# Kernel optimization log

Hardware: AMD Instinct MI355X
Metric: run time of the kernel (lower is better)

The kernel has to match this reference:

```python
import jax, jax.numpy as jnp
import numpy as np

LN_EPS = 1e-5


def setup_inputs() -> dict:
    key = jax.random.key(0)
    k1, k2, k3, k4, k5 = jax.random.split(key, 5)
    V, D_REAL, D_HID, D_MODEL = 32000, 768, 512, 4096
    B, S = 4, 2048
    return {
        "real": jax.random.normal(k1, (V, D_REAL), dtype=jnp.float32),
        "llama_embed": jax.random.normal(k2, (V, D_MODEL), dtype=jnp.float32),
        "w1": jax.random.normal(k3, (D_HID, D_REAL), dtype=jnp.float32),  # trans_1.weight
        "w2": jax.random.normal(k4, (D_MODEL, D_HID), dtype=jnp.float32),  # trans_2.weight
        "ln_w": jnp.ones((D_HID,), dtype=jnp.float32),
        "ln_b": jnp.zeros((D_HID,), dtype=jnp.float32),
        "input_ids": jax.random.randint(k5, (B, S), 0, V, dtype=jnp.int64),
    }


def _layernorm(x, w, b):
    mu = jnp.mean(x, axis=-1, keepdims=True)
    var = jnp.mean(jnp.square(x - mu), axis=-1, keepdims=True)
    return (x - mu) * jax.lax.rsqrt(var + LN_EPS) * w + b


def reference(real, llama_embed, w1, w2, ln_w, ln_b, input_ids):
    # trans_2(ELU(LayerNorm(trans_1(real)))) over the FULL table, as in the original
    h = jnp.einsum("vd,hd->vh", real, w1)            # [V, 512]
    h = jax.nn.elu(_layernorm(h, ln_w, ln_b))        # [V, 512]
    transfered = jnp.einsum("vh,mh->vm", h, w2)      # [V, 4096]
    # gather rows per token and add frozen llama embeddings
    return transfered[input_ids] + llama_embed[input_ids]  # [B, S, 4096]
```

## Files before the change

kernel.cpp:

```cpp
#include <hip/hip_runtime.h>
#include <hip/hip_bf16.h>
#include <math.h>

#define TOKENS 8192
#define D_REAL 768
#define D_HID  512
#define D_MODEL 4096

typedef __attribute__((ext_vector_type(8))) short bf16x8;
typedef __attribute__((ext_vector_type(4))) float f32x4;

__device__ inline unsigned short f2bf(float f) {
    union { float f; unsigned u; } v; v.f = f;
    unsigned r = v.u + 0x7FFFu + ((v.u >> 16) & 1u);
    return (unsigned short)(r >> 16);
}
__device__ inline float bf2f(unsigned short h) {
    union { unsigned u; float f; } v; v.u = ((unsigned)h) << 16;
    return v.f;
}
__device__ inline bf16x8 cvt8(float4 a, float4 b) {
    bf16x8 r;
    r[0] = (short)f2bf(a.x); r[1] = (short)f2bf(a.y);
    r[2] = (short)f2bf(a.z); r[3] = (short)f2bf(a.w);
    r[4] = (short)f2bf(b.x); r[5] = (short)f2bf(b.y);
    r[6] = (short)f2bf(b.z); r[7] = (short)f2bf(b.w);
    return r;
}

__device__ inline void gload_lds16(const void* g, void* lds_wave_base) {
    __builtin_amdgcn_global_load_lds(
        (const __attribute__((address_space(1))) unsigned*)g,
        (__attribute__((address_space(3))) unsigned*)lds_wave_base,
        16, 0, 0);
}

__device__ inline void BAR() {
    asm volatile("" ::: "memory");
    __builtin_amdgcn_s_barrier();
    asm volatile("" ::: "memory");
}

__global__ __launch_bounds__(256)
void gemm1_mfma(const float* __restrict__ real, const int* __restrict__ ids,
                const unsigned short* __restrict__ B,
                unsigned short* __restrict__ C)
{
    constexpr int K = D_REAL, N = D_HID;
    __shared__ __align__(16) unsigned short As[64 * 32];
    __shared__ __align__(16) unsigned short Bs[128 * 32];
    __shared__ int sIds[64];

    const int tid = threadIdx.x;
    const int rowBase = blockIdx.x * 64;
    const int colBase = blockIdx.y * 128;

    if (tid < 64) sIds[tid] = ids[rowBase + tid];
    __syncthreads();

    const int srow = tid >> 2;
    const int scol = (tid & 3) * 8;
    const float* gA = real + (size_t)sIds[srow] * K + scol;
    const unsigned short* gB = B + (size_t)(colBase + srow) * K + scol;
    unsigned short* lB = Bs + (tid >> 6) * 512;

    const int lane = tid & 63;
    const int wv   = tid >> 6;
    const int wm   = (wv >> 1) * 32;
    const int wn   = (wv & 1) * 64;
    const int frow = lane & 15;
    const int fk   = (lane >> 4) * 8;

    f32x4 acc[2][4];
    #pragma unroll
    for (int i = 0; i < 2; i++)
        #pragma unroll
        for (int j = 0; j < 4; j++) acc[i][j] = (f32x4)0.f;

    for (int k0 = 0; k0 < K; k0 += 32) {
        gload_lds16(gB + k0,                lB);
        gload_lds16(gB + k0 + (size_t)64*K, lB + 2048);
        const float4 a0 = *reinterpret_cast<const float4*>(gA + k0);
        const float4 a1 = *reinterpret_cast<const float4*>(gA + k0 + 4);
        *reinterpret_cast<bf16x8*>(&As[srow * 32 + scol]) = cvt8(a0, a1);
        __syncthreads();

        bf16x8 af[2], bg[4];
        #pragma unroll
        for (int i = 0; i < 2; i++)
            af[i] = *reinterpret_cast<const bf16x8*>(&As[(wm + i*16 + frow) * 32 + fk]);
        #pragma unroll
        for (int j = 0; j < 4; j++)
            bg[j] = *reinterpret_cast<const bf16x8*>(&Bs[(wn + j*16 + frow) * 32 + fk]);

        #pragma unroll
        for (int i = 0; i < 2; i++)
            #pragma unroll
            for (int j = 0; j < 4; j++)
                acc[i][j] = __builtin_amdgcn_mfma_f32_16x16x32_bf16(af[i], bg[j], acc[i][j], 0, 0, 0);
        __syncthreads();
    }

    const int orow0 = wm + (lane >> 4) * 4;
    const int ocol0 = wn + frow;
    #pragma unroll
    for (int i = 0; i < 2; i++)
        #pragma unroll
        for (int r = 0; r < 4; r++) {
            unsigned short* dst = C + (size_t)(rowBase + orow0 + i*16 + r) * N + colBase + ocol0;
            #pragma unroll
            for (int j = 0; j < 4; j++)
                dst[j * 16] = f2bf(acc[i][j][r]);
        }
}

__global__ __launch_bounds__(512, 4)
void gemm2_mfma(const unsigned short* __restrict__ A,
                const unsigned short* __restrict__ B,
                const int* __restrict__ ids,
                const float* __restrict__ embed,
                float* __restrict__ C)
{
    constexpr int K = D_HID, N = D_MODEL, NKT = K / 64;
    __shared__ __align__(16) unsigned short lds2[32768];
    __shared__ int sIds[128];
    unsigned short* Alds = lds2;
    unsigned short* Blds = lds2 + 16384;

    const int f   = blockIdx.x;
    const int xcd = f & 7;
    const int idx = f >> 3;
    const int rowBase = (xcd * 8 + (idx & 7)) * 128;
    const int colBase = (idx >> 3) * 128;

    const int tid  = threadIdx.x;
    const int lane = tid & 63;
    const int wv   = tid >> 6;
    const int wr   = wv >> 2;
    const int wc   = wv & 3;
    const int frow = lane & 15;
    const int fq   = lane >> 4;

    if (tid < 128) sIds[tid] = ids[rowBase + tid];

    auto STAGE = [&](const unsigned short* Mp, unsigned short* Ml,
                     int tileBase, int kt) {
        if (kt >= NKT) return;
        unsigned short* Mb = Ml + (kt & 1) * 8192;
        #pragma unroll
        for (int u = 0; u < 2; ++u) {
            const int c    = u * 512 + tid;
            const int row  = c >> 3;
            const int slot = (c & 7) ^ (row & 7);
            const unsigned short* g = Mp + (size_t)(tileBase + row) * K
                                         + kt * 64 + slot * 8;
            gload_lds16(g, Mb + (u * 512 + wv * 64) * 8);
        }
    };
    auto LDA = [&](int buf, int mf, int kk) -> bf16x8 {
        const int row  = wr * 64 + mf * 16 + frow;
        const int slot = (kk * 4 + fq) ^ (row & 7);
        return *reinterpret_cast<const bf16x8*>(Alds + buf * 8192 + row * 64 + slot * 8);
    };
    auto LDB = [&](int buf, int nf, int kk) -> bf16x8 {
        const int row  = wc * 32 + nf * 16 + frow;
        const int slot = (kk * 4 + fq) ^ (row & 7);
        return *reinterpret_cast<const bf16x8*>(Blds + buf * 8192 + row * 64 + slot * 8);
    };

    f32x4 acc[4][2];
    #pragma unroll
    for (int i = 0; i < 4; i++)
        #pragma unroll
        for (int j = 0; j < 2; j++) acc[i][j] = (f32x4)0.f;

    STAGE(A, Alds, rowBase, 0);
    STAGE(B, Blds, colBase, 0);
    STAGE(A, Alds, rowBase, 1);
    asm volatile("s_waitcnt vmcnt(2)" ::: "memory");
    __builtin_amdgcn_s_barrier();
    asm volatile("" ::: "memory");

    #pragma unroll
    for (int kt = 0; kt < NKT; ++kt) {
        const int buf = kt & 1;
        bf16x8 af0[2][2], bg[2][2];
        #pragma unroll
        for (int i = 0; i < 2; ++i)
            #pragma unroll
            for (int kk = 0; kk < 2; ++kk)
                af0[i][kk] = LDA(buf, i, kk);
        #pragma unroll
        for (int nf = 0; nf < 2; ++nf)
            #pragma unroll
            for (int kk = 0; kk < 2; ++kk)
                bg[nf][kk] = LDB(buf, nf, kk);
        STAGE(B, Blds, colBase, kt + 1);
        BAR();
        __builtin_amdgcn_s_setprio(1);
        #pragma unroll
        for (int i = 0; i < 2; ++i)
            #pragma unroll
            for (int nf = 0; nf < 2; ++nf)
                #pragma unroll
                for (int kk = 0; kk < 2; ++kk)
                    acc[i][nf] = __builtin_amdgcn_mfma_f32_16x16x32_bf16(
                        af0[i][kk], bg[nf][kk], acc[i][nf], 0, 0, 0);
        __builtin_amdgcn_s_setprio(0);
        BAR();
        bf16x8 af1[2][2];
        #pragma unroll
        for (int i = 0; i < 2; ++i)
            #pragma unroll
            for (int kk = 0; kk < 2; ++kk)
                af1[i][kk] = LDA(buf, 2 + i, kk);
        BAR();
        STAGE(A, Alds, rowBase, kt + 2);
        __builtin_amdgcn_s_setprio(1);
        #pragma unroll
        for (int i = 0; i < 2; ++i)
            #pragma unroll
            for (int nf = 0; nf < 2; ++nf)
                #pragma unroll
                for (int kk = 0; kk < 2; ++kk)
                    acc[2 + i][nf] = __builtin_amdgcn_mfma_f32_16x16x32_bf16(
                        af1[i][kk], bg[nf][kk], acc[2 + i][nf], 0, 0, 0);
        __builtin_amdgcn_s_setprio(0);
        if (kt + 2 < NKT)      asm volatile("s_waitcnt vmcnt(2)" ::: "memory");
        else if (kt + 1 < NKT) asm volatile("s_waitcnt vmcnt(0)" ::: "memory");
        BAR();
    }

    const int ocol0 = colBase + wc * 32 + frow;
    #pragma unroll
    for (int mf = 0; mf < 4; ++mf) {
        #pragma unroll
        for (int r = 0; r < 4; ++r) {
            const int lrow = wr * 64 + mf * 16 + fq * 4 + r;
            const float* e = embed + (size_t)sIds[lrow] * N + ocol0;
            float* o = C + (size_t)(rowBase + lrow) * N + ocol0;
            #pragma unroll
            for (int nf = 0; nf < 2; ++nf)
                o[nf * 16] = acc[mf][nf][r] + e[nf * 16];
        }
    }
}

__global__ __launch_bounds__(256)
void convert2_bf16(const float* __restrict__ s1, unsigned short* __restrict__ d1, int n1,
                   const float* __restrict__ s2, unsigned short* __restrict__ d2, int n2)
{
    int i = blockIdx.x * 256 + threadIdx.x;
    const float* src; unsigned short* dst;
    if (i < n1) { src = s1; dst = d1; }
    else {
        i -= n1;
        if (i >= n2) return;
        src = s2; dst = d2;
    }
    const float4 v = reinterpret_cast<const float4*>(src)[i];
    ushort4 o;
    o.x = f2bf(v.x); o.y = f2bf(v.y); o.z = f2bf(v.z); o.w = f2bf(v.w);
    reinterpret_cast<ushort4*>(dst)[i] = o;
}

__global__ __launch_bounds__(256)
void ln_elu_bf16(unsigned short* __restrict__ H,
                 const float* __restrict__ ln_w, const float* __restrict__ ln_b)
{
    const int row = blockIdx.x * 4 + (threadIdx.x >> 6);
    const int t = threadIdx.x & 63;
    unsigned short* x = H + (size_t)row * D_HID + t * 8;

    bf16x8 v = *reinterpret_cast<const bf16x8*>(x);
    float fv[8], s = 0.f, ss = 0.f;
    #pragma unroll
    for (int j = 0; j < 8; j++) {
        fv[j] = bf2f((unsigned short)v[j]);
        s += fv[j]; ss += fv[j] * fv[j];
    }
    #pragma unroll
    for (int off = 32; off > 0; off >>= 1) {
        s  += __shfl_down(s, off);
        ss += __shfl_down(ss, off);
    }
    s = __shfl(s, 0); ss = __shfl(ss, 0);
    const float mu = s * (1.f / D_HID);
    const float var = ss * (1.f / D_HID) - mu * mu;
    const float rstd = rsqrtf(var + 1e-5f);

    const float4 w0 = *reinterpret_cast<const float4*>(ln_w + t * 8);
    const float4 w1 = *reinterpret_cast<const float4*>(ln_w + t * 8 + 4);
    const float4 b0 = *reinterpret_cast<const float4*>(ln_b + t * 8);
    const float4 b1 = *reinterpret_cast<const float4*>(ln_b + t * 8 + 4);
    const float wa[8] = { w0.x, w0.y, w0.z, w0.w, w1.x, w1.y, w1.z, w1.w };
    const float ba[8] = { b0.x, b0.y, b0.z, b0.w, b1.x, b1.y, b1.z, b1.w };

    bf16x8 o;
    #pragma unroll
    for (int j = 0; j < 8; j++) {
        float y = (fv[j] - mu) * rstd * wa[j] + ba[j];
        y = y > 0.f ? y : expm1f(y);
        o[j] = (short)f2bf(y);
    }
    *reinterpret_cast<bf16x8*>(x) = o;
}

extern "C" void kernel_launch(void* const* d_in, const int* in_sizes, int n_in,
                              void* d_out, int out_size, void* d_ws, size_t ws_size,
                              hipStream_t stream)
{
    const float* real  = (const float*)d_in[0];
    const float* embed = (const float*)d_in[1];
    const float* w1    = (const float*)d_in[2];
    const float* w2    = (const float*)d_in[3];
    const float* ln_w  = (const float*)d_in[4];
    const float* ln_b  = (const float*)d_in[5];
    const int*   ids   = (const int*)d_in[6];
    float* out = (float*)d_out;

    unsigned short* Hb  = (unsigned short*)d_ws;
    unsigned short* w1b = Hb  + (size_t)TOKENS * D_HID;
    unsigned short* w2b = w1b + (size_t)D_HID * D_REAL;

    const int n1 = D_HID * D_REAL / 4, n2 = D_MODEL * D_HID / 4;
    convert2_bf16<<<(n1 + n2 + 255) / 256, 256, 0, stream>>>(w1, w1b, n1, w2, w2b, n2);

    dim3 g1(TOKENS / 64, D_HID / 128);
    gemm1_mfma<<<g1, 256, 0, stream>>>(real, ids, w1b, Hb);

    ln_elu_bf16<<<TOKENS / 4, 256, 0, stream>>>(Hb, ln_w, ln_b);

    gemm2_mfma<<<2048, 512, 0, stream>>>(Hb, w2b, ids, embed, out);
}
```

Measured before the change: 126.1 us.

## Make gemm2 persistent over columns with whole A tile resident in LDS

Replaces the 2048-block 128x128 tiled GEMM2 with 256 blocks that each load a 64x512 A tile into LDS once and loop over 16 column tiles of a 2048-wide half, streaming only B through a double buffer. The aim is to stop re-reading A from global memory for every output tile and to cut launch and prologue overhead. In exchange, occupancy drops to one block per CU with a smaller per-wave MFMA tile, and there is a full __syncthreads every k-step, which the epilogue stores now also sit behind.

```diff
diff --git a/kernel.cpp b/kernel.cpp
--- a/kernel.cpp
+++ b/kernel.cpp
@@ -35,12 +35,6 @@
         16, 0, 0);
 }
 
-__device__ inline void BAR() {
-    asm volatile("" ::: "memory");
-    __builtin_amdgcn_s_barrier();
-    asm volatile("" ::: "memory");
-}
-
 __global__ __launch_bounds__(256)
 void gemm1_mfma(const float* __restrict__ real, const int* __restrict__ ids,
                 const unsigned short* __restrict__ B,
@@ -114,24 +108,23 @@
         }
 }
 
-__global__ __launch_bounds__(512, 4)
-void gemm2_mfma(const unsigned short* __restrict__ A,
-                const unsigned short* __restrict__ B,
-                const int* __restrict__ ids,
-                const float* __restrict__ embed,
-                float* __restrict__ C)
-{
-    constexpr int K = D_HID, N = D_MODEL, NKT = K / 64;
-    __shared__ __align__(16) unsigned short lds2[32768];
-    __shared__ int sIds[128];
-    unsigned short* Alds = lds2;
-    unsigned short* Blds = lds2 + 16384;
+__global__ __launch_bounds__(512, 1)
+void gemm2_nloop(const unsigned short* __restrict__ A,
+                 const unsigned short* __restrict__ B,
+                 const int* __restrict__ ids,
+                 const float* __restrict__ embed,
+                 float* __restrict__ C)
+{
+    constexpr int K = D_HID, N = D_MODEL, NCT = 16, NGT = NCT * 8;
+    __shared__ __align__(16) unsigned short Al[64 * 512];
+    __shared__ __align__(16) unsigned short Bl[2][128 * 64];
+    __shared__ int sIds[64];
 
     const int f   = blockIdx.x;
     const int xcd = f & 7;
-    const int idx = f >> 3;
-    const int rowBase = (xcd * 8 + (idx & 7)) * 128;
-    const int colBase = (idx >> 3) * 128;
+    const int j   = f >> 3;
+    const int rowBase = ((xcd >> 1) * 32 + j) * 64;
+    const int colHalf = (xcd & 1) * 2048;
 
     const int tid  = threadIdx.x;
     const int lane = tid & 63;
@@ -141,107 +134,90 @@
     const int frow = lane & 15;
     const int fq   = lane >> 4;
 
-    if (tid < 128) sIds[tid] = ids[rowBase + tid];
-
-    auto STAGE = [&](const unsigned short* Mp, unsigned short* Ml,
-                     int tileBase, int kt) {
-        if (kt >= NKT) return;
-        unsigned short* Mb = Ml + (kt & 1) * 8192;
+    if (tid < 64) sIds[tid] = ids[rowBase + tid];
+
+    #pragma unroll
+    for (int rr = 0; rr < 8; ++rr) {
+        const int c   = rr * 512 + tid;
+        const int row = c >> 6;
+        const int ls  = c & 63;
+        const int gs  = (ls & 56) | ((ls ^ row) & 7);
+        gload_lds16(A + (size_t)(rowBase + row) * K + gs * 8,
+                    &Al[(rr * 512 + wv * 64) * 8]);
+    }
+
+    auto STAGEB = [&](int gt) {
+        if (gt >= NGT) return;
+        const int ct = gt >> 3, kt = gt & 7;
+        unsigned short* Bb = Bl[gt & 1];
         #pragma unroll
         for (int u = 0; u < 2; ++u) {
-            const int c    = u * 512 + tid;
-            const int row  = c >> 3;
-            const int slot = (c & 7) ^ (row & 7);
-            const unsigned short* g = Mp + (size_t)(tileBase + row) * K
-                                         + kt * 64 + slot * 8;
-            gload_lds16(g, Mb + (u * 512 + wv * 64) * 8);
+            const int c   = u * 512 + tid;
+            const int row = c >> 3;
+            const int gs  = ((c & 7) ^ row) & 7;
+            gload_lds16(B + (size_t)(colHalf + ct * 128 + row) * K + kt * 64 + gs * 8,
+                        Bb + (u * 512 + wv * 64) * 8);
         }
     };
-    auto LDA = [&](int buf, int mf, int kk) -> bf16x8 {
-        const int row  = wr * 64 + mf * 16 + frow;
-        const int slot = (kk * 4 + fq) ^ (row & 7);
-        return *reinterpret_cast<const bf16x8*>(Alds + buf * 8192 + row * 64 + slot * 8);
-    };
-    auto LDB = [&](int buf, int nf, int kk) -> bf16x8 {
-        const int row  = wc * 32 + nf * 16 + frow;
-        const int slot = (kk * 4 + fq) ^ (row & 7);
-        return *reinterpret_cast<const bf16x8*>(Blds + buf * 8192 + row * 64 + slot * 8);
-    };
-
-    f32x4 acc[4][2];
-    #pragma unroll
-    for (int i = 0; i < 4; i++)
-        #pragma unroll
-        for (int j = 0; j < 2; j++) acc[i][j] = (f32x4)0.f;
-
-    STAGE(A, Alds, rowBase, 0);
-    STAGE(B, Blds, colBase, 0);
-    STAGE(A, Alds, rowBase, 1);
-    asm volatile("s_waitcnt vmcnt(2)" ::: "memory");
-    __builtin_amdgcn_s_barrier();
-    asm volatile("" ::: "memory");
-
-    #pragma unroll
-    for (int kt = 0; kt < NKT; ++kt) {
-        const int buf = kt & 1;
-        bf16x8 af0[2][2], bg[2][2];
-        #pragma unroll
-        for (int i = 0; i < 2; ++i)
-            #pragma unroll
-            for (int kk = 0; kk < 2; ++kk)
-                af0[i][kk] = LDA(buf, i, kk);
-        #pragma unroll
-        for (int nf = 0; nf < 2; ++nf)
-            #pragma unroll
-            for (int kk = 0; kk < 2; ++kk)
-                bg[nf][kk] = LDB(buf, nf, kk);
-        STAGE(B, Blds, colBase, kt + 1);
-        BAR();
-        __builtin_amdgcn_s_setprio(1);
-        #pragma unroll
-        for (int i = 0; i < 2; ++i)
+
+    STAGEB(0);
+    __syncthreads();
+
+    for (int ct = 0; ct < NCT; ++ct) {
+        f32x4 acc[2][2];
+        #pragma unroll
+        for (int i = 0; i < 2; i++)
+            #pragma unroll
+            for (int n = 0; n < 2; n++) acc[i][n] = (f32x4)0.f;
+
+        #pragma unroll
+        for (int kt = 0; kt < 8; ++kt) {
+            const int gt = ct * 8 + kt;
+            const unsigned short* Bb = Bl[gt & 1];
+            bf16x8 af[2][2], bg[2][2];
+            #pragma unroll
+            for (int mf = 0; mf < 2; ++mf)
+                #pragma unroll
+                for (int kk = 0; kk < 2; ++kk) {
+                    const int arow = wr * 32 + mf * 16 + frow;
+                    const int s = kt * 8 + ((kk * 4 + fq) ^ (arow & 7));
+                    af[mf][kk] = *reinterpret_cast<const bf16x8*>(&Al[arow * 512 + s * 8]);
+                }
             #pragma unroll
             for (int nf = 0; nf < 2; ++nf)
                 #pragma unroll
-                for (int kk = 0; kk < 2; ++kk)
-                    acc[i][nf] = __builtin_amdgcn_mfma_f32_16x16x32_bf16(
-                        af0[i][kk], bg[nf][kk], acc[i][nf], 0, 0, 0);
-        __builtin_amdgcn_s_setprio(0);
-        BAR();
-        bf16x8 af1[2][2];
-        #pragma unroll
-        for (int i = 0; i < 2; ++i)
-            #pragma unroll
-            for (int kk = 0; kk < 2; ++kk)
-                af1[i][kk] = LDA(buf, 2 + i, kk);
-        BAR();
-        STAGE(A, Alds, rowBase, kt + 2);
-        __builtin_amdgcn_s_setprio(1);
-        #pragma unroll
-        for (int i = 0; i < 2; ++i)
-            #pragma unroll
-            for (int nf = 0; nf < 2; ++nf)
+                for (int kk = 0; kk < 2; ++kk) {
+                    const int brow = wc * 32 + nf * 16 + frow;
+                    const int s = (kk * 4 + fq) ^ (brow & 7);
+                    bg[nf][kk] = *reinterpret_cast<const bf16x8*>(&Bb[brow * 64 + s * 8]);
+                }
+            STAGEB(gt + 1);
+
+            #pragma unroll
+            for (int mf = 0; mf < 2; ++mf)
                 #pragma unroll
-                for (int kk = 0; kk < 2; ++kk)
-                    acc[2 + i][nf] = __builtin_amdgcn_mfma_f32_16x16x32_bf16(
-                        af1[i][kk], bg[nf][kk], acc[2 + i][nf], 0, 0, 0);
-        __builtin_amdgcn_s_setprio(0);
-        if (kt + 2 < NKT)      asm volatile("s_waitcnt vmcnt(2)" ::: "memory");
-        else if (kt + 1 < NKT) asm volatile("s_waitcnt vmcnt(0)" ::: "memory");
-        BAR();
-    }
-
-    const int ocol0 = colBase + wc * 32 + frow;
-    #pragma unroll
-    for (int mf = 0; mf < 4; ++mf) {
-        #pragma unroll
-        for (int r = 0; r < 4; ++r) {
-            const int lrow = wr * 64 + mf * 16 + fq * 4 + r;
-            const float* e = embed + (size_t)sIds[lrow] * N + ocol0;
-            float* o = C + (size_t)(rowBase + lrow) * N + ocol0;
-            #pragma unroll
-            for (int nf = 0; nf < 2; ++nf)
-                o[nf * 16] = acc[mf][nf][r] + e[nf * 16];
+                for (int nf = 0; nf < 2; ++nf)
+                    #pragma unroll
+                    for (int kk = 0; kk < 2; ++kk)
+                        acc[mf][nf] = __builtin_amdgcn_mfma_f32_16x16x32_bf16(
+                            af[mf][kk], bg[nf][kk], acc[mf][nf], 0, 0, 0);
+
+            if (kt == 7) {
+                const int ocol = colHalf + ct * 128 + wc * 32 + frow;
+                #pragma unroll
+                for (int mf = 0; mf < 2; ++mf) {
+                    #pragma unroll
+                    for (int r = 0; r < 4; ++r) {
+                        const int lrow = wr * 32 + mf * 16 + fq * 4 + r;
+                        const float* e = embed + (size_t)sIds[lrow] * N + ocol;
+                        float* o = C + (size_t)(rowBase + lrow) * N + ocol;
+                        #pragma unroll
+                        for (int nf = 0; nf < 2; ++nf)
+                            o[nf * 16] = acc[mf][nf][r] + e[nf * 16];
+                    }
+                }
+            }
+            __syncthreads();
         }
     }
 }
@@ -331,5 +307,5 @@
 
     ln_elu_bf16<<<TOKENS / 4, 256, 0, stream>>>(Hb, ln_w, ln_b);
 
-    gemm2_mfma<<<2048, 512, 0, stream>>>(Hb, w2b, ids, embed, out);
-}
+    gemm2_nloop<<<256, 512, 0, stream>>>(Hb, w2b, ids, embed, out);
+}
```

New measurement: 152.5 us. 20.9% more time.
